# Kernel tuning notes

Measured on AMD Instinct MI355X. Metric: run time of the kernel, lower is better.

The kernel has to match this reference:

```python
import jax, jax.numpy as jnp
import numpy as np
import math

DIM = 1280
NUM_HEADS = 16
HEAD_DIM = DIM // NUM_HEADS  # 80
MLP_HIDDEN = 4 * DIM         # 5120
N = 4096
EPS = 1e-6


def setup_inputs() -> dict:
    key = jax.random.key(0)
    ks = jax.random.split(key, 12)
    s = 0.02
    inp = {
        "hidden_states": jax.random.normal(ks[0], (N, DIM), jnp.float32),
        "rotary_pos_emb": jax.random.normal(ks[1], (N, HEAD_DIM // 2), jnp.float32),
        "cu_seqlens": jnp.array([0, 1024, 2048, 3072, 4096], jnp.int32),
        "norm1_w": jnp.ones((DIM,), jnp.float32),
        "norm1_b": jnp.zeros((DIM,), jnp.float32),
        "norm2_w": jnp.ones((DIM,), jnp.float32),
        "norm2_b": jnp.zeros((DIM,), jnp.float32),
        "qkv_w": jax.random.normal(ks[2], (3 * DIM, DIM), jnp.float32) * s,
        "qkv_b": jnp.zeros((3 * DIM,), jnp.float32),
        "proj_w": jax.random.normal(ks[3], (DIM, DIM), jnp.float32) * s,
        "proj_b": jnp.zeros((DIM,), jnp.float32),
        "fc1_w": jax.random.normal(ks[4], (MLP_HIDDEN, DIM), jnp.float32) * s,
        "fc1_b": jnp.zeros((MLP_HIDDEN,), jnp.float32),
        "fc2_w": jax.random.normal(ks[5], (DIM, MLP_HIDDEN), jnp.float32) * s,
        "fc2_b": jnp.zeros((DIM,), jnp.float32),
    }
    return inp


def _layernorm(x, w, b):
    m = jnp.mean(x, axis=-1, keepdims=True)
    v = jnp.mean(jnp.square(x - m), axis=-1, keepdims=True)
    return (x - m) * jax.lax.rsqrt(v + EPS) * w + b


def _apply_rope(t, cos, sin):
    # t: [N, H, hd]; cos/sin: [N, 1, hd]
    x1 = t[..., : HEAD_DIM // 2]
    x2 = t[..., HEAD_DIM // 2:]
    rot = jnp.concatenate([-x2, x1], axis=-1)
    return t * cos + rot * sin


def _quick_gelu(x):
    return x * jax.nn.sigmoid(1.702 * x)


def reference(hidden_states, rotary_pos_emb, cu_seqlens,
              norm1_w, norm1_b, norm2_w, norm2_b,
              qkv_w, qkv_b, proj_w, proj_b,
              fc1_w, fc1_b, fc2_w, fc2_b):
    n = hidden_states.shape[0]
    # ---- attention branch (pre-norm) ----
    x = _layernorm(hidden_states, norm1_w, norm1_b)
    qkv = (x @ qkv_w.T + qkv_b).reshape(n, 3, NUM_HEADS, HEAD_DIM)
    q, k, v = qkv[:, 0], qkv[:, 1], qkv[:, 2]  # [N, H, hd]
    # rotary: freqs [N, hd//2] -> tiled cos/sin [N, 1, hd]
    cos = jnp.cos(rotary_pos_emb)
    sin = jnp.sin(rotary_pos_emb)
    cos = jnp.concatenate([cos, cos], axis=-1)[:, None, :]
    sin = jnp.concatenate([sin, sin], axis=-1)[:, None, :]
    q = _apply_rope(q, cos, sin)
    k = _apply_rope(k, cos, sin)
    # block-diagonal varlen mask from cu_seqlens via segment ids
    seg = jnp.searchsorted(cu_seqlens[1:], jnp.arange(n, dtype=cu_seqlens.dtype), side="right")
    allowed = seg[:, None] == seg[None, :]  # [N, N] bool
    scores = jnp.einsum("qhd,khd->hqk", q, k) / math.sqrt(HEAD_DIM)
    scores = jnp.where(allowed[None], scores, jnp.finfo(scores.dtype).min)
    attn = jax.nn.softmax(scores.astype(jnp.float32), axis=-1).astype(q.dtype)
    out = jnp.einsum("hqk,khd->qhd", attn, v).reshape(n, DIM)
    out = out @ proj_w.T + proj_b
    h = hidden_states + out
    # ---- MLP branch (pre-norm) ----
    y = _layernorm(h, norm2_w, norm2_b)
    y = _quick_gelu(y @ fc1_w.T + fc1_b) @ fc2_w.T + fc2_b
    return h + y
```

## Files before the change

### kernel.cpp

```cpp
#include <hip/hip_runtime.h>
#include <hip/hip_bf16.h>


typedef __bf16 bf16_t;
typedef bf16_t bf16x8 __attribute__((ext_vector_type(8)));
typedef bf16_t bf16x4 __attribute__((ext_vector_type(4)));
typedef float f32x4 __attribute__((ext_vector_type(4)));

#define DIM 1280
#define NHEADS 16
#define HDIM 80
#define MLP 5120
#define NTOK 4096
#define QKV_N 3840

#define GLOAD_LDS16(gp, lp)                                                          \
    __builtin_amdgcn_global_load_lds((const __attribute__((address_space(1))) void*)(gp), \
                                     (__attribute__((address_space(3))) void*)(lp), 16, 0, 0)

__global__ void cvt_all(const float* __restrict__ s0, const float* __restrict__ s1,
                        const float* __restrict__ s2, const float* __restrict__ s3,
                        bf16_t* __restrict__ d0, bf16_t* __restrict__ d1,
                        bf16_t* __restrict__ d2, bf16_t* __restrict__ d3,
                        int n0, int n1, int n2, int n3) {
    int q0 = n0 >> 2, q1 = n1 >> 2, q2 = n2 >> 2, q3 = n3 >> 2;
    int total = q0 + q1 + q2 + q3;
    for (int i = blockIdx.x * blockDim.x + threadIdx.x; i < total;
         i += gridDim.x * blockDim.x) {
        const float* src;
        bf16_t* dst;
        int j = i;
        if (j < q0) { src = s0; dst = d0; }
        else if ((j -= q0) < q1) { src = s1; dst = d1; }
        else if ((j -= q1) < q2) { src = s2; dst = d2; }
        else { j -= q2; src = s3; dst = d3; }
        float4 v = ((const float4*)src)[j];
        bf16x4 o;
        o[0] = (bf16_t)v.x; o[1] = (bf16_t)v.y; o[2] = (bf16_t)v.z; o[3] = (bf16_t)v.w;
        *(bf16x4*)(dst + j * 4) = o;
    }
}

__global__ __launch_bounds__(256) void ln_kernel(const float* __restrict__ x,
                                                 const float* __restrict__ w,
                                                 const float* __restrict__ b,
                                                 bf16_t* __restrict__ out) {
    int row = blockIdx.x;
    const float* xr = x + (long)row * DIM;
    float v[5];
    float s = 0.f, ss = 0.f;
#pragma unroll
    for (int j = 0; j < 5; j++) {
        v[j] = xr[j * 256 + threadIdx.x];
        s += v[j];
        ss += v[j] * v[j];
    }
#pragma unroll
    for (int off = 32; off > 0; off >>= 1) {
        s += __shfl_xor(s, off, 64);
        ss += __shfl_xor(ss, off, 64);
    }
    __shared__ float red[8];
    int wid = threadIdx.x >> 6;
    if ((threadIdx.x & 63) == 0) { red[wid] = s; red[wid + 4] = ss; }
    __syncthreads();
    s = red[0] + red[1] + red[2] + red[3];
    ss = red[4] + red[5] + red[6] + red[7];
    float mean = s * (1.f / DIM);
    float var = ss * (1.f / DIM) - mean * mean;
    float rstd = rsqrtf(var + 1e-6f);
    bf16_t* orow = out + (long)row * DIM;
#pragma unroll
    for (int j = 0; j < 5; j++) {
        int d = j * 256 + threadIdx.x;
        orow[d] = (bf16_t)((v[j] - mean) * rstd * w[d] + b[d]);
    }
}

__global__ __launch_bounds__(256) void prep_kernel(const bf16_t* __restrict__ qkv,
                                                   const float* __restrict__ rot,
                                                   bf16_t* __restrict__ Qd,
                                                   bf16_t* __restrict__ Kd,
                                                   bf16_t* __restrict__ Vt) {
    const float SCL = 0.11180339887498949f * 1.4426950408889634f;
    __shared__ bf16_t tv[64 * 88];
    const int tid = threadIdx.x;
    const int t0 = blockIdx.x * 64;
    const int h = blockIdx.y;

    for (int c = tid; c < 64 * 10; c += 256) {
        int tl = c / 10, a = c % 10;
        bf16x8 v = *(const bf16x8*)(qkv + (long)(t0 + tl) * QKV_N + 2 * DIM + h * HDIM + a * 8);
        *(bf16x8*)(tv + tl * 88 + a * 8) = v;
    }

    for (int c = tid; c < 64 * 10; c += 256) {
        int tl = c / 10, a = c % 10;
        long gq = (long)(t0 + tl) * QKV_N + h * HDIM + a * 4;
        bf16x4 q1 = *(const bf16x4*)(qkv + gq);
        bf16x4 q2 = *(const bf16x4*)(qkv + gq + 40);
        bf16x4 k1 = *(const bf16x4*)(qkv + gq + DIM);
        bf16x4 k2 = *(const bf16x4*)(qkv + gq + DIM + 40);
        float4 rv = *(const float4*)(rot + (long)(t0 + tl) * 40 + a * 4);
        float rr[4] = {rv.x, rv.y, rv.z, rv.w};
        bf16x4 oq1, oq2, ok1, ok2;
#pragma unroll
        for (int j = 0; j < 4; j++) {
            float c_, s_;
            __sincosf(rr[j], &s_, &c_);
            float x1 = (float)q1[j], x2 = (float)q2[j];
            oq1[j] = (bf16_t)((x1 * c_ - x2 * s_) * SCL);
            oq2[j] = (bf16_t)((x2 * c_ + x1 * s_) * SCL);
            x1 = (float)k1[j]; x2 = (float)k2[j];
            ok1[j] = (bf16_t)(x1 * c_ - x2 * s_);
            ok2[j] = (bf16_t)(x2 * c_ + x1 * s_);
        }
        long o = ((long)h * NTOK + t0 + tl) * 96 + a * 4;
        *(bf16x4*)(Qd + o) = oq1;
        *(bf16x4*)(Qd + o + 40) = oq2;
        *(bf16x4*)(Kd + o) = ok1;
        *(bf16x4*)(Kd + o + 40) = ok2;
    }
    {
        bf16x8 z;
#pragma unroll
        for (int j = 0; j < 8; j++) z[j] = (bf16_t)0.f;
        for (int c = tid; c < 64 * 2; c += 256) {
            int tl = c / 2, a = c % 2;
            long o = ((long)h * NTOK + t0 + tl) * 96 + 80 + a * 8;
            *(bf16x8*)(Qd + o) = z;
            *(bf16x8*)(Kd + o) = z;
        }
    }
    __syncthreads();

    for (int c = tid; c < 80 * 8; c += 256) {
        int d = c / 8, tc = c % 8;
        bf16x8 v;
#pragma unroll
        for (int j = 0; j < 8; j++) v[j] = tv[(tc * 8 + j) * 88 + d];
        *(bf16x8*)(Vt + ((long)h * HDIM + d) * NTOK + t0 + tc * 8) = v;
    }
}

template <int EPI>
__global__ __launch_bounds__(512, 4) void gemmS(const bf16_t* __restrict__ A,
                                                const bf16_t* __restrict__ B,
                                                const float* __restrict__ bias,
                                                const float* __restrict__ res,
                                                void* __restrict__ Cv,
                                                int M, int N, int K, int kspl) {
    __shared__ char lds[3 * 16384];
    const int tid = threadIdx.x;
    const int lane = tid & 63;
    const int l15 = lane & 15;
    const int g = lane >> 4;
    const int wid = tid >> 6;
    const int wr = wid >> 2;
    const int wc = wid & 3;

    const int nx = gridDim.x;
    const int id = blockIdx.y * nx + blockIdx.x;
    const int cpx = (nx * gridDim.y) >> 3;
    const int sid = (id & 7) * cpx + (id >> 3);
    const int m0 = (sid / nx) * 128;
    const int n0 = (sid % nx) * 128;
    const int k0 = blockIdx.z * kspl;
    const int NT = kspl >> 5;

    const int soff = tid * 16;
    const int srow = soff >> 6;
    const int scb = (soff & 63) ^ (((srow >> 1) & 3) << 4);
    const bf16_t* gA = A + (long)(m0 + srow) * K + k0 + (scb >> 1);
    const bf16_t* gB = B + (long)(n0 + srow) * K + k0 + (scb >> 1);
    const int lAo = wid * 1024;
    const int lBo = 8192 + wid * 1024;

    f32x4 acc[4][2];
#pragma unroll
    for (int i = 0; i < 4; i++)
#pragma unroll
        for (int j = 0; j < 2; j++) acc[i][j] = (f32x4){0.f, 0.f, 0.f, 0.f};

    auto stage = [&](int buf, int t) {
        char* sb = lds + buf * 16384;
        GLOAD_LDS16(gA + t * 32, sb + lAo);
        GLOAD_LDS16(gB + t * 32, sb + lBo);
    };

    stage(0, 0);
    stage(1, 1);

    int buf = 0;
    for (int t = 0; t < NT; ++t) {
        if (t < NT - 1)
            asm volatile("s_waitcnt vmcnt(2)\n\ts_barrier" ::: "memory");
        else
            asm volatile("s_waitcnt vmcnt(0)\n\ts_barrier" ::: "memory");
        if (t + 2 < NT) stage((buf + 2) % 3, t + 2);

        const char* pA = lds + buf * 16384;
        const char* pB = pA + 8192;
        bf16x8 af[4], bb[2];
#pragma unroll
        for (int m = 0; m < 4; m++) {
            int r = wr * 64 + m * 16 + l15;
            af[m] = *(const bf16x8*)(pA + r * 64 + ((g * 16) ^ (((r >> 1) & 3) << 4)));
        }
#pragma unroll
        for (int n = 0; n < 2; n++) {
            int r = wc * 32 + n * 16 + l15;
            bb[n] = *(const bf16x8*)(pB + r * 64 + ((g * 16) ^ (((r >> 1) & 3) << 4)));
        }
        __builtin_amdgcn_s_setprio(1);
#pragma unroll
        for (int m = 0; m < 4; m++)
#pragma unroll
            for (int n = 0; n < 2; n++)
                acc[m][n] = __builtin_amdgcn_mfma_f32_16x16x32_bf16(af[m], bb[n],
                                                                    acc[m][n], 0, 0, 0);
        __builtin_amdgcn_s_setprio(0);
        buf = (buf + 1) % 3;
    }

#pragma unroll
    for (int m = 0; m < 4; m++)
#pragma unroll
        for (int n = 0; n < 2; n++) {
            const int col = n0 + wc * 32 + n * 16 + l15;
            const float bv = bias[col];
#pragma unroll
            for (int rr = 0; rr < 4; rr++) {
                const int row = m0 + wr * 64 + m * 16 + g * 4 + rr;
                const long idx = (long)row * N + col;
                float val = acc[m][n][rr] + bv;
                if (EPI == 0) {
                    ((bf16_t*)Cv)[idx] = (bf16_t)val;
                } else if (EPI == 1) {
                    ((float*)Cv)[idx] = res[idx] + val;
                } else {
                    float ge = val / (1.f + __expf(-1.702f * val));
                    ((bf16_t*)Cv)[idx] = (bf16_t)ge;
                }
            }
        }
}

__global__ __launch_bounds__(256) void attn_kernel(const bf16_t* __restrict__ Qd,
                                                   const bf16_t* __restrict__ Kd,
                                                   const bf16_t* __restrict__ Vt,
                                                   const int* __restrict__ cu,
                                                   int ncu,
                                                   bf16_t* __restrict__ out) {
    __shared__ bf16_t lK[64 * 104];
    __shared__ bf16_t lV[96 * 64];
    __shared__ bf16_t lP[4 * 16 * 72];

    const int tid = threadIdx.x;
    const int lane = tid & 63;
    const int l15 = lane & 15;
    const int g = lane >> 4;
    const int wid = tid >> 6;
    const int h = blockIdx.y;
    const int q0 = blockIdx.x * 64;

    int sseg = 0;
    for (int j = 1; j < ncu - 1; j++) if (q0 >= cu[j]) sseg = j;
    const int kbeg = cu[sseg], kend = cu[sseg + 1];

    bf16x8 aq[3];
    {
        const bf16_t* qp = Qd + ((long)h * NTOK + q0 + wid * 16 + l15) * 96;
#pragma unroll
        for (int ks = 0; ks < 3; ks++)
            aq[ks] = *(const bf16x8*)(qp + ks * 32 + g * 8);
    }

    for (int c = tid; c < 16 * 8; c += 256) {
        int d = 80 + c / 8, a = c % 8;
        bf16x8 v;
#pragma unroll
        for (int j = 0; j < 8; j++) v[j] = (d == 80) ? (bf16_t)1.f : (bf16_t)0.f;
        *(bf16x8*)((char*)lV + d * 128 + ((a * 16) ^ ((d & 7) << 4))) = v;
    }

    f32x4 o[6];
#pragma unroll
    for (int n = 0; n < 6; n++) o[n] = (f32x4){0.f, 0.f, 0.f, 0.f};

    bf16x8 rK[3], rV[3];
    auto ldK = [&](int kt) {
#pragma unroll
        for (int i = 0; i < 3; i++) {
            int c = tid + i * 256;
            int row = c / 12, c16 = c % 12;
            rK[i] = *(const bf16x8*)(Kd + ((long)h * NTOK + kt + row) * 96 + c16 * 8);
        }
    };
    auto ldV = [&](int kt) {
#pragma unroll
        for (int i = 0; i < 3; i++) {
            int c = tid + i * 256;
            if (c < 640) {
                int d = c / 8, a = c % 8;
                rV[i] = *(const bf16x8*)(Vt + ((long)h * HDIM + d) * NTOK + kt + a * 8);
            }
        }
    };
    auto wrKV = [&]() {
#pragma unroll
        for (int i = 0; i < 3; i++) {
            int c = tid + i * 256;
            int row = c / 12, c16 = c % 12;
            *(bf16x8*)(lK + row * 104 + c16 * 8) = rK[i];
        }
#pragma unroll
        for (int i = 0; i < 3; i++) {
            int c = tid + i * 256;
            if (c < 640) {
                int d = c / 8, a = c % 8;
                *(bf16x8*)((char*)lV + d * 128 + ((a * 16) ^ ((d & 7) << 4))) = rV[i];
            }
        }
    };

    ldK(kbeg); ldV(kbeg);
    wrKV();
    __syncthreads();

    for (int kt = kbeg; kt < kend; kt += 64) {
        const bool more = (kt + 64 < kend);
        if (more) { ldK(kt + 64); ldV(kt + 64); }

        f32x4 s[4];
#pragma unroll
        for (int n = 0; n < 4; n++) s[n] = (f32x4){0.f, 0.f, 0.f, 0.f};
#pragma unroll
        for (int n = 0; n < 4; n++)
#pragma unroll
            for (int ks = 0; ks < 3; ks++) {
                bf16x8 kf = *(const bf16x8*)(lK + (n * 16 + l15) * 104 + ks * 32 + g * 8);
                s[n] = __builtin_amdgcn_mfma_f32_16x16x32_bf16(aq[ks], kf, s[n], 0, 0, 0);
            }

#pragma unroll
        for (int n = 0; n < 4; n++)
#pragma unroll
            for (int r = 0; r < 4; r++)
                lP[wid * 1152 + (g * 4 + r) * 72 + n * 16 + l15] = (bf16_t)exp2f(s[n][r]);

        asm volatile("s_waitcnt lgkmcnt(0)" ::: "memory");
        bf16x8 pa[2];
#pragma unroll
        for (int ks = 0; ks < 2; ks++)
            pa[ks] = *(const bf16x8*)(lP + wid * 1152 + l15 * 72 + ks * 32 + g * 8);
#pragma unroll
        for (int n = 0; n < 6; n++)
#pragma unroll
            for (int ks = 0; ks < 2; ks++) {
                int rv = n * 16 + l15;
                bf16x8 vb = *(const bf16x8*)((char*)lV + rv * 128 +
                                             ((ks * 64 + g * 16) ^ ((rv & 7) << 4)));
                o[n] = __builtin_amdgcn_mfma_f32_16x16x32_bf16(pa[ks], vb, o[n], 0, 0, 0);
            }
        __syncthreads();
        if (more) wrKV();
        __syncthreads();
    }

    float lI[4];
#pragma unroll
    for (int r = 0; r < 4; r++) lI[r] = __shfl(o[5][r], lane & 48, 64);

#pragma unroll
    for (int n = 0; n < 5; n++)
#pragma unroll
        for (int r = 0; r < 4; r++) {
            int row = q0 + wid * 16 + g * 4 + r;
            out[(long)row * DIM + h * HDIM + n * 16 + l15] = (bf16_t)(o[n][r] / lI[r]);
        }
}

extern "C" void kernel_launch(void* const* d_in, const int* in_sizes, int n_in,
                              void* d_out, int out_size, void* d_ws, size_t ws_size,
                              hipStream_t stream) {
    const float* hidden = (const float*)d_in[0];
    const float* rot    = (const float*)d_in[1];
    const int*   cu     = (const int*)d_in[2];
    const float* n1w    = (const float*)d_in[3];
    const float* n1b    = (const float*)d_in[4];
    const float* n2w    = (const float*)d_in[5];
    const float* n2b    = (const float*)d_in[6];
    const float* qkv_w  = (const float*)d_in[7];
    const float* qkv_b  = (const float*)d_in[8];
    const float* proj_w = (const float*)d_in[9];
    const float* proj_b = (const float*)d_in[10];
    const float* fc1_w  = (const float*)d_in[11];
    const float* fc1_b  = (const float*)d_in[12];
    const float* fc2_w  = (const float*)d_in[13];
    const float* fc2_b  = (const float*)d_in[14];
    float* outp = (float*)d_out;

    char* ws = (char*)d_ws;
    bf16_t* w2   = (bf16_t*)(ws);
    bf16_t* w1   = (bf16_t*)(ws + 13107200);
    bf16_t* wp   = (bf16_t*)(ws + 26214400);
    bf16_t* wq   = (bf16_t*)(ws + 29491200);
    bf16_t* xln  = (bf16_t*)(ws + 39321600);
    bf16_t* qkvb = (bf16_t*)(ws + 49807360);
    bf16_t* Qd   = (bf16_t*)(ws + 81264640);
    bf16_t* Kd   = (bf16_t*)(ws + 93847552);
    bf16_t* Vt   = (bf16_t*)(ws + 106430464);
    bf16_t* attno= (bf16_t*)(ws + 116916224);
    bf16_t* act  = (bf16_t*)(ws + 49807360);

    int ncu = in_sizes[2];

    cvt_all<<<2048, 256, 0, stream>>>(fc2_w, fc1_w, proj_w, qkv_w,
                                      w2, w1, wp, wq,
                                      DIM * MLP, MLP * DIM, DIM * DIM, QKV_N * DIM);

    ln_kernel<<<NTOK, 256, 0, stream>>>(hidden, n1w, n1b, xln);
    gemmS<0><<<dim3(QKV_N / 128, NTOK / 128, 1), 512, 0, stream>>>(
        xln, wq, qkv_b, nullptr, qkvb, NTOK, QKV_N, DIM, DIM);
    prep_kernel<<<dim3(NTOK / 64, NHEADS), 256, 0, stream>>>(qkvb, rot, Qd, Kd, Vt);
    attn_kernel<<<dim3(NTOK / 64, NHEADS), 256, 0, stream>>>(Qd, Kd, Vt, cu, ncu, attno);
    gemmS<1><<<dim3(DIM / 128, NTOK / 128, 1), 512, 0, stream>>>(
        attno, wp, proj_b, hidden, outp, NTOK, DIM, DIM, DIM);
    ln_kernel<<<NTOK, 256, 0, stream>>>(outp, n2w, n2b, xln);
    gemmS<2><<<dim3(MLP / 128, NTOK / 128, 1), 512, 0, stream>>>(
        xln, w1, fc1_b, nullptr, act, NTOK, MLP, DIM, DIM);
    gemmS<1><<<dim3(DIM / 128, NTOK / 128, 1), 512, 0, stream>>>(
        act, w2, fc2_b, outp, outp, NTOK, DIM, MLP, MLP);
}
```

Before: 331.3 us.

## Add 128x256-tile 1024-thread GEMM for QKV and FC1 projections

Adds a new GEMM kernel gemmT that uses 128x256 output tiles with 16 waves per block and a triple-buffered LDS pipeline fed by direct global-to-LDS loads. It replaces gemmS for the QKV and FC1 GEMMs. The wider N tile is meant to raise operand reuse per loaded A tile and cut global traffic. In exchange the block count drops, so there are fewer blocks to spread across CUs, and the larger LDS footprint with 1024 threads may limit occupancy.

```diff
diff --git a/kernel.cpp b/kernel.cpp
--- a/kernel.cpp
+++ b/kernel.cpp
@@ -144,6 +144,124 @@
 }
 
 template <int EPI>
+__global__ __launch_bounds__(1024, 2) void gemmT(const bf16_t* __restrict__ A,
+                                                 const bf16_t* __restrict__ B,
+                                                 const float* __restrict__ bias,
+                                                 void* __restrict__ Cv,
+                                                 int M, int N, int K) {
+    __shared__ char lds[3 * 24576];
+    const int tid = threadIdx.x;
+    const int lane = tid & 63;
+    const int l15 = lane & 15;
+    const int g = lane >> 4;
+    const int wid = tid >> 6;
+    const int wr = wid >> 3;
+    const int wc = wid & 7;
+
+    const int nx = gridDim.x;
+    const int id = blockIdx.y * nx + blockIdx.x;
+    const int cpx = (nx * gridDim.y) >> 3;
+    const int sid = (id & 7) * cpx + (id >> 3);
+    const int m0 = (sid / nx) * 128;
+    const int n0 = (sid % nx) * 256;
+    const int NT = K >> 5;
+
+    const bf16_t* g0;
+    {
+        int off = tid * 16;
+        if (off < 8192) {
+            int row = off >> 6;
+            int cb = (off & 63) ^ (((row >> 1) & 3) << 4);
+            g0 = A + (long)(m0 + row) * K + (cb >> 1);
+        } else {
+            int b = off - 8192;
+            int row = b >> 6;
+            int cb = (b & 63) ^ (((row >> 1) & 3) << 4);
+            g0 = B + (long)(n0 + row) * K + (cb >> 1);
+        }
+    }
+    const bf16_t* g1;
+    {
+        int b = (tid & 511) * 16;
+        int row = 128 + (b >> 6);
+        int cb = (b & 63) ^ (((row >> 1) & 3) << 4);
+        g1 = B + (long)(n0 + row) * K + (cb >> 1);
+    }
+    const int l0 = wid * 1024;
+    const int l1 = 16384 + wid * 1024;
+
+    f32x4 acc[4][2];
+#pragma unroll
+    for (int i = 0; i < 4; i++)
+#pragma unroll
+        for (int j = 0; j < 2; j++) acc[i][j] = (f32x4){0.f, 0.f, 0.f, 0.f};
+
+    auto stage = [&](int buf, int t) {
+        char* sb = lds + buf * 24576;
+        GLOAD_LDS16(g0 + t * 32, sb + l0);
+        if (wid < 8) GLOAD_LDS16(g1 + t * 32, sb + l1);
+    };
+
+    stage(0, 0);
+    stage(1, 1);
+
+    int buf = 0;
+    for (int t = 0; t < NT; ++t) {
+        if (t < NT - 1) {
+            if (wid < 8) asm volatile("s_waitcnt vmcnt(2)" ::: "memory");
+            else         asm volatile("s_waitcnt vmcnt(1)" ::: "memory");
+        } else {
+            asm volatile("s_waitcnt vmcnt(0)" ::: "memory");
+        }
+        asm volatile("s_barrier" ::: "memory");
+        if (t + 2 < NT) stage((buf + 2) % 3, t + 2);
+
+        const char* pA = lds + buf * 24576;
+        const char* pB = pA + 8192;
+        bf16x8 af[4], bb[2];
+#pragma unroll
+        for (int m = 0; m < 4; m++) {
+            int r = wr * 64 + m * 16 + l15;
+            af[m] = *(const bf16x8*)(pA + r * 64 + ((g * 16) ^ (((r >> 1) & 3) << 4)));
+        }
+#pragma unroll
+        for (int n = 0; n < 2; n++) {
+            int r = wc * 32 + n * 16 + l15;
+            bb[n] = *(const bf16x8*)(pB + r * 64 + ((g * 16) ^ (((r >> 1) & 3) << 4)));
+        }
+        __builtin_amdgcn_s_setprio(1);
+#pragma unroll
+        for (int m = 0; m < 4; m++)
+#pragma unroll
+            for (int n = 0; n < 2; n++)
+                acc[m][n] = __builtin_amdgcn_mfma_f32_16x16x32_bf16(af[m], bb[n],
+                                                                    acc[m][n], 0, 0, 0);
+        __builtin_amdgcn_s_setprio(0);
+        buf = (buf + 1) % 3;
+    }
+
+#pragma unroll
+    for (int m = 0; m < 4; m++)
+#pragma unroll
+        for (int n = 0; n < 2; n++) {
+            const int col = n0 + wc * 32 + n * 16 + l15;
+            const float bv = bias[col];
+#pragma unroll
+            for (int rr = 0; rr < 4; rr++) {
+                const int row = m0 + wr * 64 + m * 16 + g * 4 + rr;
+                const long idx = (long)row * N + col;
+                float val = acc[m][n][rr] + bv;
+                if (EPI == 0) {
+                    ((bf16_t*)Cv)[idx] = (bf16_t)val;
+                } else {
+                    float ge = val / (1.f + __expf(-1.702f * val));
+                    ((bf16_t*)Cv)[idx] = (bf16_t)ge;
+                }
+            }
+        }
+}
+
+template <int EPI>
 __global__ __launch_bounds__(512, 4) void gemmS(const bf16_t* __restrict__ A,
                                                 const bf16_t* __restrict__ B,
                                                 const float* __restrict__ bias,
@@ -421,15 +539,15 @@
                                       DIM * MLP, MLP * DIM, DIM * DIM, QKV_N * DIM);
 
     ln_kernel<<<NTOK, 256, 0, stream>>>(hidden, n1w, n1b, xln);
-    gemmS<0><<<dim3(QKV_N / 128, NTOK / 128, 1), 512, 0, stream>>>(
-        xln, wq, qkv_b, nullptr, qkvb, NTOK, QKV_N, DIM, DIM);
+    gemmT<0><<<dim3(QKV_N / 256, NTOK / 128, 1), 1024, 0, stream>>>(
+        xln, wq, qkv_b, qkvb, NTOK, QKV_N, DIM);
     prep_kernel<<<dim3(NTOK / 64, NHEADS), 256, 0, stream>>>(qkvb, rot, Qd, Kd, Vt);
     attn_kernel<<<dim3(NTOK / 64, NHEADS), 256, 0, stream>>>(Qd, Kd, Vt, cu, ncu, attno);
     gemmS<1><<<dim3(DIM / 128, NTOK / 128, 1), 512, 0, stream>>>(
         attno, wp, proj_b, hidden, outp, NTOK, DIM, DIM, DIM);
     ln_kernel<<<NTOK, 256, 0, stream>>>(outp, n2w, n2b, xln);
-    gemmS<2><<<dim3(MLP / 128, NTOK / 128, 1), 512, 0, stream>>>(
-        xln, w1, fc1_b, nullptr, act, NTOK, MLP, DIM, DIM);
+    gemmT<2><<<dim3(MLP / 256, NTOK / 128, 1), 1024, 0, stream>>>(
+        xln, w1, fc1_b, act, NTOK, MLP, DIM);
     gemmS<1><<<dim3(DIM / 128, NTOK / 128, 1), 512, 0, stream>>>(
         act, w2, fc2_b, outp, outp, NTOK, DIM, MLP, MLP);
 }
```

After: 327.0 us. About the same (-1.3%).
